# Kernel optimization log

Measured on AMD Instinct MI355X. Metric: run time of the kernel, lower is better.

## Reference

```python
import jax, jax.numpy as jnp
import numpy as np

H, D, TS, A, R, TR = 256, 2, 32, 4, 16, 8  # h_size, max_output_degree, t_size, n_aggr, rank, t_rank
BS = 16384


def setup_inputs() -> dict:
    key = jax.random.key(0)
    ks = jax.random.split(key, 9)
    return {
        "neighbour_h": jax.random.normal(ks[0], (BS, D, H), jnp.float32),
        "type_embs": jax.random.normal(ks[1], (BS, TS), jnp.float32),
        # per-child input projections U: (max_output_degree, n_aggr, h_size, rank)
        "U": jax.random.normal(ks[2], (D, A, H, R), jnp.float32) * 0.05,
        "b": jax.random.normal(ks[3], (D, A, 1, R), jnp.float32) * 0.05,
        # type projection
        "U_type": jax.random.normal(ks[4], (TS, A * TR), jnp.float32) * 0.05,
        "b_type": jax.random.normal(ks[5], (1, A * TR), jnp.float32) * 0.05,
        # stacked augmented core tensors T_list: (n_aggr, t_rank+1, rank+1, rank+1, rank)
        "T": jax.random.normal(ks[6], (A, TR + 1, R + 1, R + 1, R), jnp.float32) * 0.02,
        # output projection
        "U_output": jax.random.normal(ks[7], (A, R, H), jnp.float32) * 0.05,
        "b_output": jax.random.normal(ks[8], (A, 1, H), jnp.float32) * 0.05,
    }


def _aug(x):
    # append a constant-1 feature along the last dim: (bs, a, d) -> (bs, a, d+1)
    bs, a, _ = x.shape
    return jnp.concatenate([x, jnp.ones((bs, a, 1), x.dtype)], axis=-1)


def reference(neighbour_h, type_embs, U, b, U_type, b_type, T, U_output, b_output):
    # child projections: (bs, n_ch, n_aggr, rank)
    ch = jnp.einsum('bch,cahr->bcar', neighbour_h, U) + b[:, :, 0, :]
    # type projection: (bs, n_aggr, t_rank)
    tp = (type_embs @ U_type + b_type).reshape(-1, A, TR)
    # augmented (homogeneous) inputs
    h0 = _aug(tp)         # (bs, a, TR+1)
    h1 = _aug(ch[:, 0])   # (bs, a, R+1)
    h2 = _aug(ch[:, 1])   # (bs, a, R+1)
    # sequential multilinear (Tucker/HOSVD) contraction with the core tensor,
    # vectorized over batch and aggregators (original loops over n_aggr)
    r = jnp.einsum('bap,apqrs->baqrs', h0, T)
    r = jnp.einsum('baq,baqrs->bars', h1, r)
    g = jnp.einsum('bar,bars->bas', h2, r)            # (bs, a, R)
    out = jnp.einsum('bar,arh->bah', g, U_output) + b_output[:, 0, :]
    return out.reshape(neighbour_h.shape[0], -1)      # (bs, n_aggr*h_size)
```

## Files before the change

### kernel.cpp

```cpp
#include <hip/hip_runtime.h>

#define NTHR 512
#define TB 32

typedef __attribute__((ext_vector_type(8))) short bf16x8;
typedef __attribute__((ext_vector_type(4))) float f32x4;
typedef float4 f4;
typedef unsigned short u16;

__device__ __forceinline__ u16 f2b(float x) {
  union { float f; unsigned u; } v; v.f = x;
  unsigned r = (v.u + 0x7fffu + ((v.u >> 16) & 1u)) >> 16;
  return (u16)r;
}
__device__ __forceinline__ float b2f(u16 u) {
  union { unsigned u; float f; } v; v.u = ((unsigned)u) << 16;
  return v.f;
}
__device__ __forceinline__ unsigned pack2(float a, float b) {
  return (unsigned)f2b(a) | ((unsigned)f2b(b) << 16);
}
__device__ __forceinline__ unsigned cvtpk(float lo, float hi) {
  unsigned r;
  asm("v_cvt_pk_bf16_f32 %0, %1, %2" : "=v"(r) : "v"(lo), "v"(hi));
  return r;
}
__device__ __forceinline__ float blo(unsigned u) {
  union { unsigned u; float f; } v; v.u = u << 16; return v.f;
}
__device__ __forceinline__ float bhi(unsigned u) {
  union { unsigned u; float f; } v; v.u = u & 0xffff0000u; return v.f;
}

extern "C" __global__ void hosvd_prep(const float* __restrict__ U,
                                      const float* __restrict__ T,
                                      const float* __restrict__ UO,
                                      unsigned* __restrict__ ws32) {
  int id = blockIdx.x * 256 + threadIdx.x;
  if (id < 92160) {
    int j2 = id & 3, frag = id >> 2;
    int l = frag & 63, f2 = frag >> 6;
    int p = f2 % 9, akt = f2 / 9;
    int kt = akt % 10, a = akt / 10;
    int s = l & 15;
    float v[2];
    #pragma unroll
    for (int j = 0; j < 2; ++j) {
      int kp = kt * 32 + (l >> 4) * 8 + j2 * 2 + j;
      float x = 0.f;
      if (kp < 306) {
        int q = (unsigned)kp / 18u, r = kp - q * 18;
        if (r < 17) x = T[(((a * 9 + p) * 17 + q) * 17 + r) * 16 + s];
      }
      v[j] = x;
    }
    ws32[id] = pack2(v[0], v[1]);
  } else if (id < 108544) {
    int rel = id - 92160;
    int j2 = rel & 3, frag = rel >> 2;
    int l = frag & 63, f2 = frag >> 6;
    int kt = f2 & 7, g = f2 >> 3;
    int a = g & 3, c = g >> 2;
    int rr = l & 15;
    int k = kt * 32 + (l >> 4) * 8 + j2 * 2;
    float v0 = U[((c * 4 + a) * 256 + k + 0) * 16 + rr];
    float v1 = U[((c * 4 + a) * 256 + k + 1) * 16 + rr];
    ws32[id] = pack2(v0, v1);
  } else if (id < 124928) {
    int rel = id - 108544;
    int j2 = rel & 3, frag = rel >> 2;
    int l = frag & 63, f2 = frag >> 6;
    int ht = f2 & 15, a = f2 >> 4;
    int h = ht * 16 + (l & 15);
    int k = (l >> 4) * 8 + j2 * 2;
    float v0 = (k + 0 < 16) ? UO[(a * 16 + k + 0) * 256 + h] : 0.f;
    float v1 = (k + 1 < 16) ? UO[(a * 16 + k + 1) * 256 + h] : 0.f;
    ws32[id] = pack2(v0, v1);
  }
}

#define MFMA_B(A, B, C) __builtin_amdgcn_mfma_f32_16x16x32_bf16(A, B, C, 0, 0, 0)

#define LOADB(ktv)                                                          \
  do {                                                                      \
    const u16* bp_ = &BTf[(size_t)((a * 10 + (ktv)) * 9) * 512 + l * 8];    \
    Bv0 = *(const bf16x8*)(bp_ + 0 * 512);                                  \
    Bv1 = *(const bf16x8*)(bp_ + 1 * 512);                                  \
    Bv2 = *(const bf16x8*)(bp_ + 2 * 512);                                  \
    Bv3 = *(const bf16x8*)(bp_ + 3 * 512);                                  \
    Bv4 = *(const bf16x8*)(bp_ + 4 * 512);                                  \
    Bv5 = *(const bf16x8*)(bp_ + 5 * 512);                                  \
    Bv6 = *(const bf16x8*)(bp_ + 6 * 512);                                  \
    Bv7 = *(const bf16x8*)(bp_ + 7 * 512);                                  \
    Bv8 = *(const bf16x8*)(bp_ + 8 * 512);                                  \
  } while (0)

#define MFMA18(ktv)                                                            \
  do {                                                                         \
    bf16x8 A0_ = *(const bf16x8*)&s_u[aL * 10496 + rl * 328 + (ktv) * 32 + 8 * q];        \
    bf16x8 A1_ = *(const bf16x8*)&s_u[aL * 10496 + (16 + rl) * 328 + (ktv) * 32 + 8 * q]; \
    acc[0][0] = MFMA_B(A0_, Bv0, acc[0][0]); acc[0][1] = MFMA_B(A1_, Bv0, acc[0][1]);     \
    acc[1][0] = MFMA_B(A0_, Bv1, acc[1][0]); acc[1][1] = MFMA_B(A1_, Bv1, acc[1][1]);     \
    acc[2][0] = MFMA_B(A0_, Bv2, acc[2][0]); acc[2][1] = MFMA_B(A1_, Bv2, acc[2][1]);     \
    acc[3][0] = MFMA_B(A0_, Bv3, acc[3][0]); acc[3][1] = MFMA_B(A1_, Bv3, acc[3][1]);     \
    acc[4][0] = MFMA_B(A0_, Bv4, acc[4][0]); acc[4][1] = MFMA_B(A1_, Bv4, acc[4][1]);     \
    acc[5][0] = MFMA_B(A0_, Bv5, acc[5][0]); acc[5][1] = MFMA_B(A1_, Bv5, acc[5][1]);     \
    acc[6][0] = MFMA_B(A0_, Bv6, acc[6][0]); acc[6][1] = MFMA_B(A1_, Bv6, acc[6][1]);     \
    acc[7][0] = MFMA_B(A0_, Bv7, acc[7][0]); acc[7][1] = MFMA_B(A1_, Bv7, acc[7][1]);     \
    acc[8][0] = MFMA_B(A0_, Bv8, acc[8][0]); acc[8][1] = MFMA_B(A1_, Bv8, acc[8][1]);     \
  } while (0)

extern "C" __global__ __launch_bounds__(NTHR, 4)
void hosvd_main(const float* __restrict__ nh, const float* __restrict__ te,
                const float* __restrict__ bw, const float* __restrict__ Ut,
                const float* __restrict__ bt, const float* __restrict__ bO,
                const u16* __restrict__ BTf, const u16* __restrict__ UcTf,
                const u16* __restrict__ UOTf, float* __restrict__ out) {
  __shared__ __align__(16) u16   s_u[20992];
  __shared__ __align__(16) u16   s_ch[TB * 164];
  __shared__ __align__(16) float s_tpt[36 * 32];
  __shared__ __align__(16) u16   s_g[TB * 136];
  __shared__ __align__(16) float s_red[3264];

  const int t = threadIdx.x;
  const int ib0 = blockIdx.x * TB;
  const int w = t >> 6, l = t & 63;
  const int rl = l & 15, q = l >> 4;

  {
    const int row = t >> 4, cc = (t >> 3) & 1, aa = (t >> 1) & 3, sl = t & 1;
    s_ch[row * 164 + cc * 80 + aa * 20 + 16 + sl] = sl ? (u16)0 : (u16)0x3F80;
  }
  if (t < 128) {
    const int aa = t >> 5, row = t & 31;
    s_tpt[(aa * 9 + 8) * 32 + row] = 1.0f;
  }

  if (t < 256) {
    const int row = t >> 3, k4 = t & 7;
    f4 v = *(const f4*)&te[(size_t)(ib0 + row) * 32 + k4 * 4];
    float* d = &s_red[row * 33 + k4 * 4];
    d[0] = v.x; d[1] = v.y; d[2] = v.z; d[3] = v.w;
  }
  for (int lp = t; lp < 4096; lp += NTHR) {
    const int row = lp >> 7, rem = lp & 127;
    const int c = rem >> 6, k0 = (rem & 63) * 4;
    f4 v = *(const f4*)&nh[((size_t)(ib0 + row) * 2 + c) * 256 + k0];
    *(uint2*)&s_u[row * 520 + c * 256 + k0] =
        make_uint2(cvtpk(v.x, v.y), cvtpk(v.z, v.w));
  }
  __syncthreads();

  {
    const int i = t >> 4, o = t & 15;
    const int off = o * 2;
    const int aa = off >> 3, p0 = off & 7;
    float acc0 = bt[off], acc1 = bt[off + 1];
    #pragma unroll
    for (int k = 0; k < 32; ++k) {
      float tv = s_red[i * 33 + k];
      float2 u = *(const float2*)&Ut[k * 32 + off];
      acc0 = fmaf(tv, u.x, acc0);
      acc1 = fmaf(tv, u.y, acc1);
    }
    s_tpt[(aa * 9 + p0) * 32 + i]     = acc0;
    s_tpt[(aa * 9 + p0 + 1) * 32 + i] = acc1;
  }

  {
    const int c = w >> 2, a = w & 3;
    const u16* u0 = &UcTf[((size_t)((c * 4 + a) * 8) * 64 + l) * 8];
    bf16x8 C0 = *(const bf16x8*)(u0 + 0 * 512);
    bf16x8 C1 = *(const bf16x8*)(u0 + 1 * 512);
    bf16x8 C2 = *(const bf16x8*)(u0 + 2 * 512);
    bf16x8 C3 = *(const bf16x8*)(u0 + 3 * 512);
    bf16x8 C4 = *(const bf16x8*)(u0 + 4 * 512);
    bf16x8 C5 = *(const bf16x8*)(u0 + 5 * 512);
    bf16x8 C6 = *(const bf16x8*)(u0 + 6 * 512);
    bf16x8 C7 = *(const bf16x8*)(u0 + 7 * 512);
    f32x4 ac0 = {0.f, 0.f, 0.f, 0.f}, ac1 = {0.f, 0.f, 0.f, 0.f};
    #define PCKT(KT, CB)                                                          \
    {                                                                             \
      bf16x8 A0_ = *(const bf16x8*)&s_u[rl * 520 + c * 256 + KT * 32 + 8 * q];    \
      bf16x8 A1_ = *(const bf16x8*)&s_u[(16 + rl) * 520 + c * 256 + KT * 32 + 8 * q]; \
      ac0 = MFMA_B(A0_, CB, ac0);                                                 \
      ac1 = MFMA_B(A1_, CB, ac1);                                                 \
    }
    PCKT(0, C0) PCKT(1, C1) PCKT(2, C2) PCKT(3, C3)
    PCKT(4, C4) PCKT(5, C5) PCKT(6, C6) PCKT(7, C7)
    #undef PCKT
    const float bias = bw[(c * 4 + a) * 16 + rl];
    #pragma unroll
    for (int reg = 0; reg < 4; ++reg) {
      s_ch[(4 * q + reg) * 164 + c * 80 + a * 20 + rl]      = f2b(ac0[reg] + bias);
      s_ch[(16 + 4 * q + reg) * 164 + c * 80 + a * 20 + rl] = f2b(ac1[reg] + bias);
    }
  }
  __syncthreads();

  const int aL = w >> 2;
  const int kq = w & 3;
  const int kt0 = (kq <= 2) ? kq * 3 : 8;
  const int ktn = (kq < 2) ? 3 : 2;

  for (int it = 0; it < 2; ++it) {
    const int aB = it * 2;
    const int a = aB + aL;

    bf16x8 Bv0, Bv1, Bv2, Bv3, Bv4, Bv5, Bv6, Bv7, Bv8;
    LOADB(kt0);

    for (int lp = t; lp < 1152; lp += NTHR) {
      const int row = lp & 31, rest = lp >> 5;
      const int aLb = (rest >= 18) ? 1 : 0;
      const int qv = rest - aLb * 18;
      const int ab = aB + aLb;
      const float h1f = b2f(s_ch[row * 164 + ab * 20 + qv]);
      const u16* h2p = &s_ch[row * 164 + 80 + ab * 20];
      uint2 ha = *(const uint2*)&h2p[0];
      uint2 hb = *(const uint2*)&h2p[4];
      uint2 hc = *(const uint2*)&h2p[8];
      uint2 hd = *(const uint2*)&h2p[12];
      unsigned he = *(const unsigned*)&h2p[16];
      unsigned* op = (unsigned*)&s_u[aLb * 10496 + row * 328 + qv * 18];
      op[0] = cvtpk(h1f * blo(ha.x), h1f * bhi(ha.x));
      op[1] = cvtpk(h1f * blo(ha.y), h1f * bhi(ha.y));
      op[2] = cvtpk(h1f * blo(hb.x), h1f * bhi(hb.x));
      op[3] = cvtpk(h1f * blo(hb.y), h1f * bhi(hb.y));
      op[4] = cvtpk(h1f * blo(hc.x), h1f * bhi(hc.x));
      op[5] = cvtpk(h1f * blo(hc.y), h1f * bhi(hc.y));
      op[6] = cvtpk(h1f * blo(hd.x), h1f * bhi(hd.x));
      op[7] = cvtpk(h1f * blo(hd.y), h1f * bhi(hd.y));
      op[8] = cvtpk(h1f * blo(he),   h1f * bhi(he));
    }
    __syncthreads();

    f32x4 acc[9][2];
    #pragma unroll
    for (int p = 0; p < 9; ++p) {
      acc[p][0] = (f32x4){0.f, 0.f, 0.f, 0.f};
      acc[p][1] = (f32x4){0.f, 0.f, 0.f, 0.f};
    }
    __builtin_amdgcn_s_setprio(1);
    MFMA18(kt0);
    for (int kk = 1; kk < ktn; ++kk) {
      LOADB(kt0 + kk);
      MFMA18(kt0 + kk);
    }
    __builtin_amdgcn_s_setprio(0);

    float gp[2][4] = {{0.f, 0.f, 0.f, 0.f}, {0.f, 0.f, 0.f, 0.f}};
    #pragma unroll
    for (int p = 0; p < 9; ++p) {
      #pragma unroll
      for (int mm = 0; mm < 2; ++mm) {
        f4 tv = *(const f4*)&s_tpt[(a * 9 + p) * 32 + mm * 16 + 4 * q];
        gp[mm][0] = fmaf(tv.x, acc[p][mm][0], gp[mm][0]);
        gp[mm][1] = fmaf(tv.y, acc[p][mm][1], gp[mm][1]);
        gp[mm][2] = fmaf(tv.z, acc[p][mm][2], gp[mm][2]);
        gp[mm][3] = fmaf(tv.w, acc[p][mm][3], gp[mm][3]);
      }
    }
    if (kq) {
      #pragma unroll
      for (int mm = 0; mm < 2; ++mm)
        #pragma unroll
        for (int reg = 0; reg < 4; ++reg)
          s_red[((kq - 1) * 2 + aL) * 544 + mm * 272 + (4 * q + reg) * 17 + rl] =
              gp[mm][reg];
    }
    __syncthreads();

    if (kq == 0) {
      #pragma unroll
      for (int mm = 0; mm < 2; ++mm)
        #pragma unroll
        for (int reg = 0; reg < 4; ++reg) {
          const int idx = aL * 544 + mm * 272 + (4 * q + reg) * 17 + rl;
          float g = gp[mm][reg] + s_red[idx] + s_red[1088 + idx] + s_red[2176 + idx];
          const int row = mm * 16 + 4 * q + reg;
          s_g[row * 136 + a * 32 + rl]      = f2b(g);
          s_g[row * 136 + a * 32 + 16 + rl] = 0;
        }
    }
  }
  __syncthreads();

  {
    const int e = w;
    #pragma unroll
    for (int a = 0; a < 4; ++a) {
      const u16* ub = &UOTf[((size_t)(a * 16 + e * 2) * 64 + l) * 8];
      bf16x8 E0 = *(const bf16x8*)(ub);
      bf16x8 E1 = *(const bf16x8*)(ub + 512);
      bf16x8 A0 = *(const bf16x8*)&s_g[rl * 136 + a * 32 + 8 * q];
      bf16x8 A1 = *(const bf16x8*)&s_g[(16 + rl) * 136 + a * 32 + 8 * q];
      const float b0 = bO[a * 256 + (e * 2 + 0) * 16 + rl];
      const float b1 = bO[a * 256 + (e * 2 + 1) * 16 + rl];
      f32x4 e00 = {b0, b0, b0, b0}, e01 = e00;
      f32x4 e10 = {b1, b1, b1, b1}, e11 = e10;
      e00 = MFMA_B(A0, E0, e00);
      e01 = MFMA_B(A1, E0, e01);
      e10 = MFMA_B(A0, E1, e10);
      e11 = MFMA_B(A1, E1, e11);
      #pragma unroll
      for (int reg = 0; reg < 4; ++reg) {
        const size_t r0 = (size_t)(ib0 + 4 * q + reg) * 1024 + a * 256;
        const size_t r1 = (size_t)(ib0 + 16 + 4 * q + reg) * 1024 + a * 256;
        out[r0 + (e * 2 + 0) * 16 + rl] = e00[reg];
        out[r1 + (e * 2 + 0) * 16 + rl] = e01[reg];
        out[r0 + (e * 2 + 1) * 16 + rl] = e10[reg];
        out[r1 + (e * 2 + 1) * 16 + rl] = e11[reg];
      }
    }
  }
}

extern "C" void kernel_launch(void* const* d_in, const int* in_sizes, int n_in,
                              void* d_out, int out_size, void* d_ws, size_t ws_size,
                              hipStream_t stream) {
  const float* nh = (const float*)d_in[0];
  const float* te = (const float*)d_in[1];
  const float* U  = (const float*)d_in[2];
  const float* bw = (const float*)d_in[3];
  const float* Ut = (const float*)d_in[4];
  const float* bt = (const float*)d_in[5];
  const float* T  = (const float*)d_in[6];
  const float* UO = (const float*)d_in[7];
  const float* bO = (const float*)d_in[8];
  float* out = (float*)d_out;

  unsigned* ws32 = (unsigned*)d_ws;
  hipLaunchKernelGGL(hosvd_prep, dim3(488), dim3(256), 0, stream, U, T, UO, ws32);

  const u16* BTf  = (const u16*)d_ws;
  const u16* UcTf = BTf + 184320;
  const u16* UOTf = UcTf + 32768;

  const int bs = in_sizes[0] / 512;
  hipLaunchKernelGGL(hosvd_main, dim3(bs / TB), dim3(NTHR), 0, stream,
                     nh, te, bw, Ut, bt, bO, BTf, UcTf, UOTf, out);
}
```

Before: 42.59 us.

## Reorder core-tensor GEMM loops to stream B fragments and fold type weights per slice

```diff
diff --git a/kernel.cpp b/kernel.cpp
--- a/kernel.cpp
+++ b/kernel.cpp
@@ -81,33 +81,53 @@
 
 #define MFMA_B(A, B, C) __builtin_amdgcn_mfma_f32_16x16x32_bf16(A, B, C, 0, 0, 0)
 
-#define LOADB(ktv)                                                          \
-  do {                                                                      \
-    const u16* bp_ = &BTf[(size_t)((a * 10 + (ktv)) * 9) * 512 + l * 8];    \
-    Bv0 = *(const bf16x8*)(bp_ + 0 * 512);                                  \
-    Bv1 = *(const bf16x8*)(bp_ + 1 * 512);                                  \
-    Bv2 = *(const bf16x8*)(bp_ + 2 * 512);                                  \
-    Bv3 = *(const bf16x8*)(bp_ + 3 * 512);                                  \
-    Bv4 = *(const bf16x8*)(bp_ + 4 * 512);                                  \
-    Bv5 = *(const bf16x8*)(bp_ + 5 * 512);                                  \
-    Bv6 = *(const bf16x8*)(bp_ + 6 * 512);                                  \
-    Bv7 = *(const bf16x8*)(bp_ + 7 * 512);                                  \
-    Bv8 = *(const bf16x8*)(bp_ + 8 * 512);                                  \
+#define LOADP(DST, P, KTN)                                                   \
+  do {                                                                       \
+    _Pragma("unroll")                                                        \
+    for (int kk = 0; kk < (KTN); ++kk)                                       \
+      DST[kk] = *(const bf16x8*)&BTf[(size_t)((a * 10 + kt0 + kk) * 9 + (P)) * 512 + l * 8]; \
   } while (0)
 
-#define MFMA18(ktv)                                                            \
-  do {                                                                         \
-    bf16x8 A0_ = *(const bf16x8*)&s_u[aL * 10496 + rl * 328 + (ktv) * 32 + 8 * q];        \
-    bf16x8 A1_ = *(const bf16x8*)&s_u[aL * 10496 + (16 + rl) * 328 + (ktv) * 32 + 8 * q]; \
-    acc[0][0] = MFMA_B(A0_, Bv0, acc[0][0]); acc[0][1] = MFMA_B(A1_, Bv0, acc[0][1]);     \
-    acc[1][0] = MFMA_B(A0_, Bv1, acc[1][0]); acc[1][1] = MFMA_B(A1_, Bv1, acc[1][1]);     \
-    acc[2][0] = MFMA_B(A0_, Bv2, acc[2][0]); acc[2][1] = MFMA_B(A1_, Bv2, acc[2][1]);     \
-    acc[3][0] = MFMA_B(A0_, Bv3, acc[3][0]); acc[3][1] = MFMA_B(A1_, Bv3, acc[3][1]);     \
-    acc[4][0] = MFMA_B(A0_, Bv4, acc[4][0]); acc[4][1] = MFMA_B(A1_, Bv4, acc[4][1]);     \
-    acc[5][0] = MFMA_B(A0_, Bv5, acc[5][0]); acc[5][1] = MFMA_B(A1_, Bv5, acc[5][1]);     \
-    acc[6][0] = MFMA_B(A0_, Bv6, acc[6][0]); acc[6][1] = MFMA_B(A1_, Bv6, acc[6][1]);     \
-    acc[7][0] = MFMA_B(A0_, Bv7, acc[7][0]); acc[7][1] = MFMA_B(A1_, Bv7, acc[7][1]);     \
-    acc[8][0] = MFMA_B(A0_, Bv8, acc[8][0]); acc[8][1] = MFMA_B(A1_, Bv8, acc[8][1]);     \
+#define DOP(BSET, P, KTN)                                                    \
+  do {                                                                       \
+    f32x4 c0_ = {0.f, 0.f, 0.f, 0.f}, c1_ = {0.f, 0.f, 0.f, 0.f};            \
+    _Pragma("unroll")                                                        \
+    for (int kk = 0; kk < (KTN); ++kk) {                                     \
+      c0_ = MFMA_B(Af0[kk], BSET[kk], c0_);                                  \
+      c1_ = MFMA_B(Af1[kk], BSET[kk], c1_);                                  \
+    }                                                                        \
+    f4 tv0_ = *(const f4*)&s_tpt[(a * 9 + (P)) * 32 + 4 * q];                \
+    f4 tv1_ = *(const f4*)&s_tpt[(a * 9 + (P)) * 32 + 16 + 4 * q];           \
+    gp0[0] = fmaf(tv0_.x, c0_[0], gp0[0]);                                   \
+    gp0[1] = fmaf(tv0_.y, c0_[1], gp0[1]);                                   \
+    gp0[2] = fmaf(tv0_.z, c0_[2], gp0[2]);                                   \
+    gp0[3] = fmaf(tv0_.w, c0_[3], gp0[3]);                                   \
+    gp1[0] = fmaf(tv1_.x, c1_[0], gp1[0]);                                   \
+    gp1[1] = fmaf(tv1_.y, c1_[1], gp1[1]);                                   \
+    gp1[2] = fmaf(tv1_.z, c1_[2], gp1[2]);                                   \
+    gp1[3] = fmaf(tv1_.w, c1_[3], gp1[3]);                                   \
+  } while (0)
+
+#define CORE_GEMM(KTN)                                                       \
+  do {                                                                       \
+    const u16* oa_ = &s_u[aL * 10496];                                       \
+    bf16x8 Af0[KTN], Af1[KTN];                                               \
+    _Pragma("unroll")                                                        \
+    for (int kk = 0; kk < (KTN); ++kk) {                                     \
+      Af0[kk] = *(const bf16x8*)&oa_[rl * 328 + (kt0 + kk) * 32 + 8 * q];    \
+      Af1[kk] = *(const bf16x8*)&oa_[(16 + rl) * 328 + (kt0 + kk) * 32 + 8 * q]; \
+    }                                                                        \
+    bf16x8 Ba[KTN], Bb[KTN], Bc[KTN];                                        \
+    LOADP(Ba, 0, KTN); LOADP(Bb, 1, KTN); LOADP(Bc, 2, KTN);                 \
+    DOP(Ba, 0, KTN); LOADP(Ba, 3, KTN);                                      \
+    DOP(Bb, 1, KTN); LOADP(Bb, 4, KTN);                                      \
+    DOP(Bc, 2, KTN); LOADP(Bc, 5, KTN);                                      \
+    DOP(Ba, 3, KTN); LOADP(Ba, 6, KTN);                                      \
+    DOP(Bb, 4, KTN); LOADP(Bb, 7, KTN);                                      \
+    DOP(Bc, 5, KTN); LOADP(Bc, 8, KTN);                                      \
+    DOP(Ba, 6, KTN);                                                         \
+    DOP(Bb, 7, KTN);                                                         \
+    DOP(Bc, 8, KTN);                                                         \
   } while (0)
 
 extern "C" __global__ __launch_bounds__(NTHR, 4)
@@ -141,6 +161,9 @@
     f4 v = *(const f4*)&te[(size_t)(ib0 + row) * 32 + k4 * 4];
     float* d = &s_red[row * 33 + k4 * 4];
     d[0] = v.x; d[1] = v.y; d[2] = v.z; d[3] = v.w;
+  } else {
+    const int j = t - 256;
+    *(f4*)&s_red[1056 + j * 4] = *(const f4*)&Ut[j * 4];
   }
   for (int lp = t; lp < 4096; lp += NTHR) {
     const int row = lp >> 7, rem = lp & 127;
@@ -159,7 +182,7 @@
     #pragma unroll
     for (int k = 0; k < 32; ++k) {
       float tv = s_red[i * 33 + k];
-      float2 u = *(const float2*)&Ut[k * 32 + off];
+      float2 u = *(const float2*)&s_red[1056 + k * 32 + off];
       acc0 = fmaf(tv, u.x, acc0);
       acc1 = fmaf(tv, u.y, acc1);
     }
@@ -201,14 +224,10 @@
   const int aL = w >> 2;
   const int kq = w & 3;
   const int kt0 = (kq <= 2) ? kq * 3 : 8;
-  const int ktn = (kq < 2) ? 3 : 2;
 
   for (int it = 0; it < 2; ++it) {
     const int aB = it * 2;
     const int a = aB + aL;
-
-    bf16x8 Bv0, Bv1, Bv2, Bv3, Bv4, Bv5, Bv6, Bv7, Bv8;
-    LOADB(kt0);
 
     for (int lp = t; lp < 1152; lp += NTHR) {
       const int row = lp & 31, rest = lp >> 5;
@@ -235,39 +254,17 @@
     }
     __syncthreads();
 
-    f32x4 acc[9][2];
-    #pragma unroll
-    for (int p = 0; p < 9; ++p) {
-      acc[p][0] = (f32x4){0.f, 0.f, 0.f, 0.f};
-      acc[p][1] = (f32x4){0.f, 0.f, 0.f, 0.f};
-    }
+    f32x4 gp0 = {0.f, 0.f, 0.f, 0.f}, gp1 = {0.f, 0.f, 0.f, 0.f};
     __builtin_amdgcn_s_setprio(1);
-    MFMA18(kt0);
-    for (int kk = 1; kk < ktn; ++kk) {
-      LOADB(kt0 + kk);
-      MFMA18(kt0 + kk);
-    }
+    if (kq < 2) { CORE_GEMM(3); } else { CORE_GEMM(2); }
     __builtin_amdgcn_s_setprio(0);
 
-    float gp[2][4] = {{0.f, 0.f, 0.f, 0.f}, {0.f, 0.f, 0.f, 0.f}};
-    #pragma unroll
-    for (int p = 0; p < 9; ++p) {
-      #pragma unroll
-      for (int mm = 0; mm < 2; ++mm) {
-        f4 tv = *(const f4*)&s_tpt[(a * 9 + p) * 32 + mm * 16 + 4 * q];
-        gp[mm][0] = fmaf(tv.x, acc[p][mm][0], gp[mm][0]);
-        gp[mm][1] = fmaf(tv.y, acc[p][mm][1], gp[mm][1]);
-        gp[mm][2] = fmaf(tv.z, acc[p][mm][2], gp[mm][2]);
-        gp[mm][3] = fmaf(tv.w, acc[p][mm][3], gp[mm][3]);
-      }
-    }
     if (kq) {
       #pragma unroll
-      for (int mm = 0; mm < 2; ++mm)
-        #pragma unroll
-        for (int reg = 0; reg < 4; ++reg)
-          s_red[((kq - 1) * 2 + aL) * 544 + mm * 272 + (4 * q + reg) * 17 + rl] =
-              gp[mm][reg];
+      for (int reg = 0; reg < 4; ++reg) {
+        s_red[((kq - 1) * 2 + aL) * 544 + (4 * q + reg) * 17 + rl]       = gp0[reg];
+        s_red[((kq - 1) * 2 + aL) * 544 + 272 + (4 * q + reg) * 17 + rl] = gp1[reg];
+      }
     }
     __syncthreads();
 
@@ -277,7 +274,8 @@
         #pragma unroll
         for (int reg = 0; reg < 4; ++reg) {
           const int idx = aL * 544 + mm * 272 + (4 * q + reg) * 17 + rl;
-          float g = gp[mm][reg] + s_red[idx] + s_red[1088 + idx] + s_red[2176 + idx];
+          float g = (mm ? gp1[reg] : gp0[reg]) +
+                    s_red[idx] + s_red[1088 + idx] + s_red[2176 + idx];
           const int row = mm * 16 + 4 * q + reg;
           s_g[row * 136 + a * 32 + rl]      = f2b(g);
           s_g[row * 136 + a * 32 + 16 + rl] = 0;
```

Result: slower. 44.33 us (+4.1%).
